# Optimization experiments

Measured on AMD Instinct MI355X. Metric: run time of the kernel, lower is better.

## Reference

```python
import jax, jax.numpy as jnp
import numpy as np

N, IN, OUT, H = 4096, 512, 64, 8
ALPHA = 0.2
NEG = -9e15


def glorot(key, shape):
    fan_in, fan_out = shape[-2], shape[-1]
    limit = np.sqrt(6.0 / (fan_in + fan_out))
    return jax.random.uniform(key, shape, jnp.float32, -limit, limit)


def setup_inputs() -> dict:
    key = jax.random.key(0)
    k1, k2, k3, k4, k5 = jax.random.split(key, 5)
    x = jax.random.normal(k1, (N, IN), jnp.float32)
    adj = jax.random.randint(k2, (N, N), 0, 2, jnp.int32)
    W = glorot(k3, (H, IN, OUT))            # stacked per-head kernels
    a1 = glorot(k4, (H, OUT, 1))[..., 0]    # [H, OUT] self attn vec
    a2 = glorot(k5, (H, OUT, 1))[..., 0]    # [H, OUT] neigh attn vec
    return {"x": x, "adj": adj, "W": W, "a1": a1, "a2": a2}


def reference(x, adj, W, a1, a2):
    # Wh: [H, N, OUT]
    Wh = jnp.einsum("ni,hio->hno", x, W)
    f1 = jnp.einsum("hno,ho->hn", Wh, a1)  # [H, N]
    f2 = jnp.einsum("hno,ho->hn", Wh, a2)  # [H, N]
    e = jax.nn.leaky_relu(f1[:, :, None] + f2[:, None, :], ALPHA)  # [H, N, N]
    e = jnp.where(adj[None] > 0, e, NEG)
    attn = jax.nn.softmax(e, axis=-1)       # dropout inactive (eval mode)
    h = jnp.einsum("hnm,hmo->hno", attn, Wh)  # [H, N, OUT]
    # concat heads along features -> [N, H*OUT]
    out = jnp.transpose(h, (1, 0, 2)).reshape(N, H * OUT)
    return out
```

## Files before the change

kernel.cpp:

```cpp
#include <hip/hip_runtime.h>
#include <hip/hip_bf16.h>
#include <stdint.h>


constexpr int N_ = 4096, IN_ = 512, OUT_ = 64, H_ = 8;
constexpr float ALPHA_ = 0.2f;

typedef __attribute__((ext_vector_type(8))) short short8;
typedef __attribute__((ext_vector_type(4))) float f32x4;

__device__ __forceinline__ uint32_t rne_pack2(float a, float b, float& ra, float& rb) {
    uint32_t ua = __float_as_uint(a); ua += 0x7fffu + ((ua >> 16) & 1u); ua >>= 16;
    uint32_t ub = __float_as_uint(b); ub += 0x7fffu + ((ub >> 16) & 1u); ub >>= 16;
    ra = __uint_as_float(ua << 16);
    rb = __uint_as_float(ub << 16);
    return ua | (ub << 16);
}

__global__ __launch_bounds__(256) void pack_adj(const int* __restrict__ adj,
                                                unsigned long long* __restrict__ bitsT) {
    size_t g = (size_t)blockIdx.x * 256 + threadIdx.x;
    int v = adj[g];
    unsigned long long m = __ballot(v != 0);
    if ((threadIdx.x & 63) == 0) {
        int n = (int)(g >> 12);
        int c = (int)((g >> 6) & 63);
        bitsT[(size_t)c * N_ + n] = m;
    }
}

__global__ __launch_bounds__(256) void split_x(const float* __restrict__ x,
                                               uint16_t* __restrict__ xh,
                                               uint16_t* __restrict__ xl) {
    size_t g = ((size_t)blockIdx.x * 256 + threadIdx.x) * 8;
    float4 v0 = *(const float4*)(x + g);
    float4 v1 = *(const float4*)(x + g + 4);
    float v[8] = {v0.x, v0.y, v0.z, v0.w, v1.x, v1.y, v1.z, v1.w};
    uint32_t ph[4], pl[4];
#pragma unroll
    for (int i = 0; i < 4; i++) {
        float h0, h1, d0, d1;
        ph[i] = rne_pack2(v[2 * i], v[2 * i + 1], h0, h1);
        pl[i] = rne_pack2(v[2 * i] - h0, v[2 * i + 1] - h1, d0, d1);
    }
    *(uint4*)(xh + g) = make_uint4(ph[0], ph[1], ph[2], ph[3]);
    *(uint4*)(xl + g) = make_uint4(pl[0], pl[1], pl[2], pl[3]);
}

__global__ __launch_bounds__(256) void split_wT(const float* __restrict__ W,
                                                uint16_t* __restrict__ WTh,
                                                uint16_t* __restrict__ WTl) {
    __shared__ float T[64 * 68];
    const int t  = threadIdx.x;
    const int kb = blockIdx.x;
    const int h  = blockIdx.y;
    {
        int kk = t >> 2, os = (t & 3) * 16;
        const float* src = W + ((size_t)h * IN_ + kb * 64 + kk) * OUT_ + os;
#pragma unroll
        for (int j = 0; j < 4; j++)
            *(float4*)&T[kk * 68 + os + j * 4] = *(const float4*)(src + j * 4);
    }
    __syncthreads();
    int o = t >> 2, ks = (t & 3) * 16;
    uint32_t ph[8], pl[8];
#pragma unroll
    for (int i = 0; i < 8; i++) {
        float va = T[(ks + 2 * i) * 68 + o], vb = T[(ks + 2 * i + 1) * 68 + o];
        float h0, h1, d0, d1;
        ph[i] = rne_pack2(va, vb, h0, h1);
        pl[i] = rne_pack2(va - h0, vb - h1, d0, d1);
    }
    size_t dst = ((size_t)h * OUT_ + o) * IN_ + kb * 64 + ks;
    *(uint4*)&WTh[dst]     = make_uint4(ph[0], ph[1], ph[2], ph[3]);
    *(uint4*)&WTh[dst + 8] = make_uint4(ph[4], ph[5], ph[6], ph[7]);
    *(uint4*)&WTl[dst]     = make_uint4(pl[0], pl[1], pl[2], pl[3]);
    *(uint4*)&WTl[dst + 8] = make_uint4(pl[4], pl[5], pl[6], pl[7]);
}

__global__ __launch_bounds__(256) void wh_mfma(const uint16_t* __restrict__ xh,
                                               const uint16_t* __restrict__ xl,
                                               const uint16_t* __restrict__ WTh,
                                               const uint16_t* __restrict__ WTl,
                                               const float* __restrict__ a1,
                                               const float* __restrict__ a2,
                                               uint16_t* __restrict__ WhhT,
                                               float* __restrict__ f1,
                                               float* __restrict__ f2) {
    __shared__ __align__(16) char ldsbuf[4 * 64 * 72 * 2];
    uint16_t* Ah = (uint16_t*)ldsbuf;
    uint16_t* Al = Ah + 64 * 72;
    uint16_t* Bh = Al + 64 * 72;
    uint16_t* Bl = Bh + 64 * 72;
    const int t  = threadIdx.x;
    const int h  = blockIdx.y;
    const int n0 = blockIdx.x * 64;
    const int l  = t & 63, w = t >> 6;
    const int p  = l & 15, q = l >> 4;
    const int sr = t >> 2, sc = (t & 3) * 16;

    f32x4 acc[4];
#pragma unroll
    for (int rt = 0; rt < 4; rt++) acc[rt] = (f32x4){0.f, 0.f, 0.f, 0.f};

    const uint16_t* gxh = xh + (size_t)(n0 + sr) * IN_ + sc;
    const uint16_t* gxl = xl + (size_t)(n0 + sr) * IN_ + sc;
    const uint16_t* gbh = WTh + ((size_t)h * OUT_ + sr) * IN_ + sc;
    const uint16_t* gbl = WTl + ((size_t)h * OUT_ + sr) * IN_ + sc;

    for (int kt = 0; kt < 8; kt++) {
        __syncthreads();
        uint4 a0 = *(const uint4*)(gxh + kt * 64);
        uint4 a1v = *(const uint4*)(gxh + kt * 64 + 8);
        uint4 b0 = *(const uint4*)(gxl + kt * 64);
        uint4 b1 = *(const uint4*)(gxl + kt * 64 + 8);
        uint4 c0 = *(const uint4*)(gbh + kt * 64);
        uint4 c1 = *(const uint4*)(gbh + kt * 64 + 8);
        uint4 d0 = *(const uint4*)(gbl + kt * 64);
        uint4 d1 = *(const uint4*)(gbl + kt * 64 + 8);
        *(uint4*)&Ah[sr * 72 + sc]     = a0;
        *(uint4*)&Ah[sr * 72 + sc + 8] = a1v;
        *(uint4*)&Al[sr * 72 + sc]     = b0;
        *(uint4*)&Al[sr * 72 + sc + 8] = b1;
        *(uint4*)&Bh[sr * 72 + sc]     = c0;
        *(uint4*)&Bh[sr * 72 + sc + 8] = c1;
        *(uint4*)&Bl[sr * 72 + sc]     = d0;
        *(uint4*)&Bl[sr * 72 + sc + 8] = d1;
        __syncthreads();
#pragma unroll
        for (int k0 = 0; k0 < 2; k0++) {
            short8 bhf = *(const short8*)&Bh[(w * 16 + p) * 72 + q * 8 + k0 * 32];
            short8 blf = *(const short8*)&Bl[(w * 16 + p) * 72 + q * 8 + k0 * 32];
#pragma unroll
            for (int rt = 0; rt < 4; rt++) {
                short8 ahf = *(const short8*)&Ah[(rt * 16 + p) * 72 + q * 8 + k0 * 32];
                short8 alf = *(const short8*)&Al[(rt * 16 + p) * 72 + q * 8 + k0 * 32];
                acc[rt] = __builtin_amdgcn_mfma_f32_16x16x32_bf16(ahf, bhf, acc[rt], 0, 0, 0);
                acc[rt] = __builtin_amdgcn_mfma_f32_16x16x32_bf16(alf, bhf, acc[rt], 0, 0, 0);
                acc[rt] = __builtin_amdgcn_mfma_f32_16x16x32_bf16(ahf, blf, acc[rt], 0, 0, 0);
            }
        }
    }
    __syncthreads();
    float* Whs = (float*)ldsbuf;
#pragma unroll
    for (int rt = 0; rt < 4; rt++)
#pragma unroll
        for (int reg = 0; reg < 4; reg++)
            Whs[(rt * 16 + q * 4 + reg) * 68 + w * 16 + p] = acc[rt][reg];
    __syncthreads();
    {
        int r = t >> 2, og = (t & 3) * 16;
        float s1 = 0.f, s2 = 0.f;
#pragma unroll
        for (int j = 0; j < 4; j++) {
            float4 wv = *(const float4*)&Whs[r * 68 + og + j * 4];
            float4 av = *(const float4*)(a1 + h * OUT_ + og + j * 4);
            float4 bv = *(const float4*)(a2 + h * OUT_ + og + j * 4);
            s1 += wv.x * av.x + wv.y * av.y + wv.z * av.z + wv.w * av.w;
            s2 += wv.x * bv.x + wv.y * bv.y + wv.z * bv.z + wv.w * bv.w;
        }
        s1 += __shfl_xor(s1, 1, 64); s1 += __shfl_xor(s1, 2, 64);
        s2 += __shfl_xor(s2, 1, 64); s2 += __shfl_xor(s2, 2, 64);
        if ((t & 3) == 0) {
            f1[(size_t)h * N_ + n0 + r] = s1;
            f2[(size_t)h * N_ + n0 + r] = s2;
        }
    }
    {
        int o = t >> 2, ns = (t & 3) * 16;
        uint32_t ph[8];
#pragma unroll
        for (int i = 0; i < 8; i++) {
            float va = Whs[(ns + 2 * i) * 68 + o], vb = Whs[(ns + 2 * i + 1) * 68 + o];
            float h0, h1;
            ph[i] = rne_pack2(va, vb, h0, h1);
        }
        size_t dst = ((size_t)h * OUT_ + o) * N_ + n0 + ns;
        *(uint4*)&WhhT[dst]     = make_uint4(ph[0], ph[1], ph[2], ph[3]);
        *(uint4*)&WhhT[dst + 8] = make_uint4(ph[4], ph[5], ph[6], ph[7]);
    }
}

__global__ __launch_bounds__(256, 4) void gat_main(const unsigned long long* __restrict__ bitsT,
                                                   const uint16_t* __restrict__ WhhT,
                                                   const float* __restrict__ f1,
                                                   const float* __restrict__ f2,
                                                   float* __restrict__ outNum,
                                                   float* __restrict__ op1,
                                                   float* __restrict__ Lpart) {
    __shared__ __align__(16) uint16_t Bh[2][64 * 72];
    const int t  = threadIdx.x;
    const int h  = blockIdx.y, z = blockIdx.z;
    const int n0 = blockIdx.x * 64;
    const int l  = t & 63, w = t >> 6;
    const int p  = l & 15, q = l >> 4;
    const int sr = t >> 2, sc = (t & 3) * 16;
    const int row = w * 16 + p;

    const float f1v = f1[(size_t)h * N_ + n0 + row];
    const float* f2b = f2 + (size_t)h * N_ + (size_t)z * 2048;
    const uint16_t* gb = WhhT + ((size_t)h * OUT_ + sr) * N_ + (size_t)z * 2048 + sc;
    const unsigned long long* bptr = bitsT + (size_t)(z * 32) * N_ + n0 + row;

    float Lp = 0.f;
    f32x4 acc[4];
#pragma unroll
    for (int ct = 0; ct < 4; ct++) acc[ct] = (f32x4){0.f, 0.f, 0.f, 0.f};

    {
        uint4 b0 = *(const uint4*)(gb);
        uint4 b1 = *(const uint4*)(gb + 8);
        *(uint4*)&Bh[0][sr * 72 + sc]     = b0;
        *(uint4*)&Bh[0][sr * 72 + sc + 8] = b1;
    }
    unsigned long long word = bptr[0];

    for (int cc = 0; cc < 32; cc++) {
        uint16_t* Bcur = Bh[cc & 1];
        uint16_t* Bnxt = Bh[(cc & 1) ^ 1];
        __syncthreads();
        uint4 nb0 = *(const uint4*)(gb + (cc + 1) * 64);
        uint4 nb1 = *(const uint4*)(gb + (cc + 1) * 64 + 8);
        unsigned long long nword = bptr[(size_t)(cc + 1) * N_];
        const float* fpc = f2b + cc * 64 + q * 8;
        float4 fa0 = *(const float4*)(fpc);
        float4 fa1 = *(const float4*)(fpc + 4);
        float4 fb0 = *(const float4*)(fpc + 32);
        float4 fb1 = *(const float4*)(fpc + 36);
#pragma unroll
        for (int k0 = 0; k0 < 2; k0++) {
            float fs[8];
            if (k0 == 0) {
                fs[0] = fa0.x; fs[1] = fa0.y; fs[2] = fa0.z; fs[3] = fa0.w;
                fs[4] = fa1.x; fs[5] = fa1.y; fs[6] = fa1.z; fs[7] = fa1.w;
            } else {
                fs[0] = fb0.x; fs[1] = fb0.y; fs[2] = fb0.z; fs[3] = fb0.w;
                fs[4] = fb1.x; fs[5] = fb1.y; fs[6] = fb1.z; fs[7] = fb1.w;
            }
            uint32_t bits8 = (uint32_t)(word >> (k0 * 32 + q * 8)) & 0xffu;
            float pv[8];
#pragma unroll
            for (int j = 0; j < 8; j++) {
                float s = f1v + fs[j];
                float e = fmaxf(s, ALPHA_ * s);
                float ex = __expf(e);
                pv[j] = ((bits8 >> j) & 1u) ? ex : 0.f;
            }
            union { short8 s8; uint32_t u[4]; } af;
#pragma unroll
            for (int i = 0; i < 4; i++) {
                uint32_t pk;
                asm("v_cvt_pk_bf16_f32 %0, %1, %2"
                    : "=v"(pk)
                    : "v"(pv[2 * i]), "v"(pv[2 * i + 1]));
                af.u[i] = pk;
                Lp += __uint_as_float(pk << 16) + __uint_as_float(pk & 0xffff0000u);
            }
#pragma unroll
            for (int ct = 0; ct < 4; ct++) {
                short8 bhf = *(const short8*)&Bcur[(ct * 16 + p) * 72 + q * 8 + k0 * 32];
                acc[ct] = __builtin_amdgcn_mfma_f32_16x16x32_bf16(af.s8, bhf, acc[ct], 0, 0, 0);
            }
        }
        *(uint4*)&Bnxt[sr * 72 + sc]     = nb0;
        *(uint4*)&Bnxt[sr * 72 + sc + 8] = nb1;
        word = nword;
    }
    float Ls = Lp;
    Ls += __shfl_xor(Ls, 16, 64);
    Ls += __shfl_xor(Ls, 32, 64);
    if (q == 0) Lpart[((size_t)z * 8 + h) * N_ + n0 + row] = Ls;
    float* dst = (z == 0) ? outNum : op1;
#pragma unroll
    for (int ct = 0; ct < 4; ct++)
#pragma unroll
        for (int reg = 0; reg < 4; reg++) {
            int rr = w * 16 + q * 4 + reg;
            dst[(size_t)(n0 + rr) * (H_ * OUT_) + h * OUT_ + ct * 16 + p] = acc[ct][reg];
        }
}

__global__ __launch_bounds__(256) void combine(float* __restrict__ outb,
                                               const float* __restrict__ op1,
                                               const float* __restrict__ Lpart) {
    size_t g = (size_t)blockIdx.x * 256 + threadIdx.x;
    int n = (int)(g >> 7);
    int c = (int)(g & 127);
    int h = c >> 4;
    float4 o0 = ((const float4*)outb)[g];
    float4 o1 = ((const float4*)op1)[g];
    float L = Lpart[(size_t)h * N_ + n] + Lpart[(size_t)(8 + h) * N_ + n];
    float inv = 1.f / L;
    ((float4*)outb)[g] = make_float4((o0.x + o1.x) * inv, (o0.y + o1.y) * inv,
                                     (o0.z + o1.z) * inv, (o0.w + o1.w) * inv);
}

extern "C" void kernel_launch(void* const* d_in, const int* in_sizes, int n_in,
                              void* d_out, int out_size, void* d_ws, size_t ws_size,
                              hipStream_t stream) {
    const float* x   = nullptr;
    const int*   adj = nullptr;
    const float* W   = nullptr;
    const float* a1  = nullptr;
    const float* a2  = nullptr;
    for (int i = 0; i < n_in; i++) {
        long long sz = in_sizes[i];
        if      (sz == (long long)N_ * IN_)        x   = (const float*)d_in[i];
        else if (sz == (long long)N_ * N_)         adj = (const int*)d_in[i];
        else if (sz == (long long)H_ * IN_ * OUT_) W   = (const float*)d_in[i];
        else if (sz == (long long)H_ * OUT_) {
            if (!a1) a1 = (const float*)d_in[i];
            else     a2 = (const float*)d_in[i];
        }
    }
    if (!x)   x   = (const float*)d_in[0];
    if (!adj) adj = (const int*)d_in[1];
    if (!W)   W   = (const float*)d_in[2];
    if (!a1)  a1  = (const float*)d_in[3];
    if (!a2)  a2  = (const float*)d_in[4];
    float* out = (float*)d_out;

    char* ws = (char*)d_ws;
    unsigned long long* bitsT = (unsigned long long*)ws;
    uint16_t* WhhT = (uint16_t*)(ws + (2u  << 20));
    float* f1      = (float*)   (ws + (6u  << 20));
    float* f2      = (float*)   (ws + (6u  << 20) + (128u << 10));
    float* Lpart   = (float*)   (ws + (6u  << 20) + (256u << 10));
    float* op1     = (float*)   (ws + (6u  << 20) + (512u << 10));
    uint16_t* xh   = (uint16_t*)(ws + (6u  << 20) + (512u << 10));
    uint16_t* xl   = (uint16_t*)(ws + (10u << 20) + (512u << 10));
    uint16_t* WTh  = (uint16_t*)(ws + (14u << 20) + (512u << 10));
    uint16_t* WTl  = (uint16_t*)(ws + (15u << 20));

    pack_adj<<<(N_ * (size_t)N_) / 256, 256, 0, stream>>>(adj, bitsT);
    split_x<<<(N_ * IN_) / (256 * 8), 256, 0, stream>>>(x, xh, xl);
    split_wT<<<dim3(IN_ / 64, H_), 256, 0, stream>>>(W, WTh, WTl);
    wh_mfma<<<dim3(N_ / 64, H_), 256, 0, stream>>>(xh, xl, WTh, WTl, a1, a2, WhhT, f1, f2);
    gat_main<<<dim3(N_ / 64, H_, 2), 256, 0, stream>>>(bitsT, WhhT, f1, f2, out, op1, Lpart);
    combine<<<(N_ * H_ * OUT_) / (256 * 4), 256, 0, stream>>>(out, op1, Lpart);
}
```

Before: 203.1 us.

## Fuse split-K combine into gat_main via in-block LDS reduction; grid-stride pack_adj

gat_main now runs both key halves in one 512-thread block, two 256-thread groups, and reduces the partial numerators and softmax denominators through shared memory. It then writes the normalized output directly, so the separate combine kernel and the op1/Lpart round trip through global memory go away. pack_adj is changed to a 16-iteration grid-stride loop with fewer blocks, and the mask select becomes a bitwise AND. The cost is halved block count for gat_main at larger blocks plus extra barriers and LDS traffic for the reduction.

After: 201.4 us. About the same (-0.8%).

```diff
diff --git a/kernel.cpp b/kernel.cpp
--- a/kernel.cpp
+++ b/kernel.cpp
@@ -19,13 +19,18 @@
 
 __global__ __launch_bounds__(256) void pack_adj(const int* __restrict__ adj,
                                                 unsigned long long* __restrict__ bitsT) {
-    size_t g = (size_t)blockIdx.x * 256 + threadIdx.x;
-    int v = adj[g];
-    unsigned long long m = __ballot(v != 0);
-    if ((threadIdx.x & 63) == 0) {
-        int n = (int)(g >> 12);
-        int c = (int)((g >> 6) & 63);
-        bitsT[(size_t)c * N_ + n] = m;
+    size_t base = (size_t)blockIdx.x * 256 + threadIdx.x;
+    const size_t stride = (size_t)4096 * 256;
+#pragma unroll
+    for (int it = 0; it < 16; it++) {
+        size_t g = base + (size_t)it * stride;
+        int v = adj[g];
+        unsigned long long m = __ballot(v != 0);
+        if ((threadIdx.x & 63) == 0) {
+            int n = (int)(g >> 12);
+            int c = (int)((g >> 6) & 63);
+            bitsT[(size_t)c * N_ + n] = m;
+        }
     }
 }
 
@@ -182,26 +187,27 @@
     }
 }
 
-__global__ __launch_bounds__(256, 4) void gat_main(const unsigned long long* __restrict__ bitsT,
+__global__ __launch_bounds__(512, 4) void gat_main(const unsigned long long* __restrict__ bitsT,
                                                    const uint16_t* __restrict__ WhhT,
                                                    const float* __restrict__ f1,
                                                    const float* __restrict__ f2,
-                                                   float* __restrict__ outNum,
-                                                   float* __restrict__ op1,
-                                                   float* __restrict__ Lpart) {
-    __shared__ __align__(16) uint16_t Bh[2][64 * 72];
-    const int t  = threadIdx.x;
-    const int h  = blockIdx.y, z = blockIdx.z;
-    const int n0 = blockIdx.x * 64;
-    const int l  = t & 63, w = t >> 6;
-    const int p  = l & 15, q = l >> 4;
-    const int sr = t >> 2, sc = (t & 3) * 16;
-    const int row = w * 16 + p;
+                                                   float* __restrict__ out) {
+    __shared__ __align__(16) uint16_t Bh[2][2][64 * 72];
+    const int t   = threadIdx.x;
+    const int h   = blockIdx.y;
+    const int n0  = blockIdx.x * 64;
+    const int grp = t >> 8;
+    const int tg  = t & 255;
+    const int l   = t & 63;
+    const int wg  = tg >> 6;
+    const int p   = l & 15, q = l >> 4;
+    const int sr  = tg >> 2, sc = (tg & 3) * 16;
+    const int row = wg * 16 + p;
 
     const float f1v = f1[(size_t)h * N_ + n0 + row];
-    const float* f2b = f2 + (size_t)h * N_ + (size_t)z * 2048;
-    const uint16_t* gb = WhhT + ((size_t)h * OUT_ + sr) * N_ + (size_t)z * 2048 + sc;
-    const unsigned long long* bptr = bitsT + (size_t)(z * 32) * N_ + n0 + row;
+    const float* f2b = f2 + (size_t)h * N_ + (size_t)grp * 2048;
+    const uint16_t* gb = WhhT + ((size_t)h * OUT_ + sr) * N_ + (size_t)grp * 2048 + sc;
+    const unsigned long long* bp = bitsT + (size_t)(grp * 32) * N_ + n0 + row;
 
     float Lp = 0.f;
     f32x4 acc[4];
@@ -211,18 +217,20 @@
     {
         uint4 b0 = *(const uint4*)(gb);
         uint4 b1 = *(const uint4*)(gb + 8);
-        *(uint4*)&Bh[0][sr * 72 + sc]     = b0;
-        *(uint4*)&Bh[0][sr * 72 + sc + 8] = b1;
-    }
-    unsigned long long word = bptr[0];
+        *(uint4*)&Bh[grp][0][sr * 72 + sc]     = b0;
+        *(uint4*)&Bh[grp][0][sr * 72 + sc + 8] = b1;
+    }
+    unsigned long long word = bp[0];
+    bp += N_;
 
     for (int cc = 0; cc < 32; cc++) {
-        uint16_t* Bcur = Bh[cc & 1];
-        uint16_t* Bnxt = Bh[(cc & 1) ^ 1];
+        uint16_t* Bcur = Bh[grp][cc & 1];
+        uint16_t* Bnxt = Bh[grp][(cc & 1) ^ 1];
         __syncthreads();
         uint4 nb0 = *(const uint4*)(gb + (cc + 1) * 64);
         uint4 nb1 = *(const uint4*)(gb + (cc + 1) * 64 + 8);
-        unsigned long long nword = bptr[(size_t)(cc + 1) * N_];
+        unsigned long long nword = *bp;
+        bp += N_;
         const float* fpc = f2b + cc * 64 + q * 8;
         float4 fa0 = *(const float4*)(fpc);
         float4 fa1 = *(const float4*)(fpc + 4);
@@ -245,7 +253,8 @@
                 float s = f1v + fs[j];
                 float e = fmaxf(s, ALPHA_ * s);
                 float ex = __expf(e);
-                pv[j] = ((bits8 >> j) & 1u) ? ex : 0.f;
+                uint32_t msk = (uint32_t)((int32_t)(bits8 << (31 - j)) >> 31);
+                pv[j] = __uint_as_float(__float_as_uint(ex) & msk);
             }
             union { short8 s8; uint32_t u[4]; } af;
 #pragma unroll
@@ -270,30 +279,36 @@
     float Ls = Lp;
     Ls += __shfl_xor(Ls, 16, 64);
     Ls += __shfl_xor(Ls, 32, 64);
-    if (q == 0) Lpart[((size_t)z * 8 + h) * N_ + n0 + row] = Ls;
-    float* dst = (z == 0) ? outNum : op1;
-#pragma unroll
-    for (int ct = 0; ct < 4; ct++)
+
+    __syncthreads();
+    float* Red  = (float*)&Bh[0][0][0];
+    float* Lsum = Red + 128;
+    if (q == 0) Red[grp * 64 + row] = Ls;
+    if (grp == 1) {
+#pragma unroll
+        for (int ct = 0; ct < 4; ct++)
+#pragma unroll
+            for (int reg = 0; reg < 4; reg++)
+                Lsum[(wg * 16 + q * 4 + reg) * 68 + ct * 16 + p] = acc[ct][reg];
+    }
+    __syncthreads();
+    if (grp == 0) {
+        float inv[4];
 #pragma unroll
         for (int reg = 0; reg < 4; reg++) {
-            int rr = w * 16 + q * 4 + reg;
-            dst[(size_t)(n0 + rr) * (H_ * OUT_) + h * OUT_ + ct * 16 + p] = acc[ct][reg];
-        }
-}
-
-__global__ __launch_bounds__(256) void combine(float* __restrict__ outb,
-                                               const float* __restrict__ op1,
-                                               const float* __restrict__ Lpart) {
-    size_t g = (size_t)blockIdx.x * 256 + threadIdx.x;
-    int n = (int)(g >> 7);
-    int c = (int)(g & 127);
-    int h = c >> 4;
-    float4 o0 = ((const float4*)outb)[g];
-    float4 o1 = ((const float4*)op1)[g];
-    float L = Lpart[(size_t)h * N_ + n] + Lpart[(size_t)(8 + h) * N_ + n];
-    float inv = 1.f / L;
-    ((float4*)outb)[g] = make_float4((o0.x + o1.x) * inv, (o0.y + o1.y) * inv,
-                                     (o0.z + o1.z) * inv, (o0.w + o1.w) * inv);
+            int rr = wg * 16 + q * 4 + reg;
+            float L = Red[rr] + Red[64 + rr];
+            inv[reg] = 1.f / L;
+        }
+#pragma unroll
+        for (int ct = 0; ct < 4; ct++)
+#pragma unroll
+            for (int reg = 0; reg < 4; reg++) {
+                int rr = wg * 16 + q * 4 + reg;
+                float v = (acc[ct][reg] + Lsum[rr * 68 + ct * 16 + p]) * inv[reg];
+                out[(size_t)(n0 + rr) * (H_ * OUT_) + h * OUT_ + ct * 16 + p] = v;
+            }
+    }
 }
 
 extern "C" void kernel_launch(void* const* d_in, const int* in_sizes, int n_in,
@@ -326,17 +341,14 @@
     uint16_t* WhhT = (uint16_t*)(ws + (2u  << 20));
     float* f1      = (float*)   (ws + (6u  << 20));
     float* f2      = (float*)   (ws + (6u  << 20) + (128u << 10));
-    float* Lpart   = (float*)   (ws + (6u  << 20) + (256u << 10));
-    float* op1     = (float*)   (ws + (6u  << 20) + (512u << 10));
     uint16_t* xh   = (uint16_t*)(ws + (6u  << 20) + (512u << 10));
     uint16_t* xl   = (uint16_t*)(ws + (10u << 20) + (512u << 10));
     uint16_t* WTh  = (uint16_t*)(ws + (14u << 20) + (512u << 10));
     uint16_t* WTl  = (uint16_t*)(ws + (15u << 20));
 
-    pack_adj<<<(N_ * (size_t)N_) / 256, 256, 0, stream>>>(adj, bitsT);
+    pack_adj<<<4096, 256, 0, stream>>>(adj, bitsT);
     split_x<<<(N_ * IN_) / (256 * 8), 256, 0, stream>>>(x, xh, xl);
     split_wT<<<dim3(IN_ / 64, H_), 256, 0, stream>>>(W, WTh, WTl);
     wh_mfma<<<dim3(N_ / 64, H_), 256, 0, stream>>>(xh, xl, WTh, WTl, a1, a2, WhhT, f1, f2);
-    gat_main<<<dim3(N_ / 64, H_, 2), 256, 0, stream>>>(bitsT, WhhT, f1, f2, out, op1, Lpart);
-    combine<<<(N_ * H_ * OUT_) / (256 * 4), 256, 0, stream>>>(out, op1, Lpart);
-}
+    gat_main<<<dim3(N_ / 64, H_), 512, 0, stream>>>(bitsT, WhhT, f1, f2, out);
+}
```
